# Kernel optimization log

Hardware: AMD Instinct MI355X
Metric: run time of the kernel (lower is better)

## Reference

```python
import jax, jax.numpy as jnp
import numpy as np

NUM_HEADS = 16


def setup_inputs() -> dict:
    key = jax.random.key(0)
    k1, k2, k3 = jax.random.split(key, 3)
    B, N, D = 4, 1024, 1024
    x = jax.random.normal(k1, (B, N, D), dtype=jnp.float32)
    w_qkv = jax.random.normal(k2, (3 * D, D), dtype=jnp.float32) * (D ** -0.5)
    w_out = jax.random.normal(k3, (D, D), dtype=jnp.float32) * (D ** -0.5)
    b_out = jnp.zeros((D,), dtype=jnp.float32)
    return {"x": x, "w_qkv": w_qkv, "w_out": w_out, "b_out": b_out}


def reference(x, w_qkv, w_out, b_out):
    B, N, D = x.shape
    H = NUM_HEADS
    d = D // H
    scale = d ** -0.5
    # qkv projection (no bias): [B,N,3D] -> [B,N,3,H,d]
    qkv = jnp.einsum('bnd,ed->bne', x, w_qkv).reshape(B, N, 3, H, d)
    # -> [3, B, H, N, d]
    qkv = jnp.transpose(qkv, (2, 0, 3, 1, 4))
    q, k, v = qkv[0], qkv[1], qkv[2]
    # attention scores [B,H,N,N], stable softmax
    scores = jnp.einsum('bhqd,bhkd->bhqk', q, k) * scale
    attn = jax.nn.softmax(scores, axis=-1)
    out = jnp.einsum('bhqk,bhkd->bhqd', attn, v)  # [B,H,N,d]
    out = jnp.transpose(out, (0, 2, 1, 3)).reshape(B, N, D)
    # output projection with bias
    return jnp.einsum('bnd,ed->bne', out, w_out) + b_out
```

## Files before the change

### kernel.cpp

```cpp
#include <hip/hip_runtime.h>
#include <stdint.h>

typedef __bf16 bf16_t;
typedef bf16_t bf16x8 __attribute__((ext_vector_type(8)));
typedef float f32x4 __attribute__((ext_vector_type(4)));

static __device__ __forceinline__ unsigned short f2bf(float f) {
    union { float f; unsigned int u; } v; v.f = f;
    unsigned int u = v.u;
    unsigned int r = (u + 0x7fffu + ((u >> 16) & 1u)) >> 16;
    return (unsigned short)r;
}

static __device__ __forceinline__ bf16x8 as_frag(uint4 v) {
    union { uint4 u; bf16x8 b; } c; c.u = v; return c.b;
}

static __device__ __forceinline__ void gl2lds16(const unsigned short* g, uint4* l) {
    __builtin_amdgcn_global_load_lds(
        (const __attribute__((address_space(1))) unsigned int*)g,
        (__attribute__((address_space(3))) unsigned int*)l, 16, 0, 0);
}

#define MFMA16(a, b, c) __builtin_amdgcn_mfma_f32_16x16x32_bf16((a), (b), (c), 0, 0, 0)

__global__ void cvt_all(const float* __restrict__ x,
                        const float* __restrict__ wq,
                        const float* __restrict__ wo,
                        unsigned short* __restrict__ xb,
                        unsigned short* __restrict__ wqb,
                        unsigned short* __restrict__ wob) {
    const float* in; unsigned short* out; int n4;
    if (blockIdx.y == 0)      { in = x;  out = xb;  n4 = 1048576; }
    else if (blockIdx.y == 1) { in = wq; out = wqb; n4 = 786432; }
    else                      { in = wo; out = wob; n4 = 262144; }
    for (int i = blockIdx.x * 256 + threadIdx.x; i < n4; i += 1024 * 256) {
        float4 v = ((const float4*)in)[i];
        ushort4 o;
        o.x = f2bf(v.x); o.y = f2bf(v.y); o.z = f2bf(v.z); o.w = f2bf(v.w);
        ((ushort4*)out)[i] = o;
    }
}

template <int OUTMODE>
__global__ __launch_bounds__(256, 2) void gemm_bt(
    const unsigned short* __restrict__ A,
    const unsigned short* __restrict__ B,
    void* __restrict__ Cv,
    const float* __restrict__ bias,
    unsigned short* __restrict__ Vt,
    int M, int N, int K) {
    __shared__ uint4 As[1024];
    __shared__ uint4 Bs[1024];
    const int tid  = threadIdx.x;
    const int lane = tid & 63;
    const int wave = tid >> 6;
    const int quad = lane >> 4;
    const int l16  = lane & 15;
    const int wr   = (wave >> 1) * 64;
    const int wc   = (wave & 1) * 64;
    const int bm   = blockIdx.y * 128;
    const int bn   = blockIdx.x * 128;

    f32x4 zero4 = {0.f, 0.f, 0.f, 0.f};
    f32x4 acc[4][4];
#pragma unroll
    for (int mt = 0; mt < 4; ++mt)
#pragma unroll
        for (int nt = 0; nt < 4; ++nt) acc[mt][nt] = zero4;

    const int s_row = tid >> 3;
    const int s_kcs = tid & 7;

    for (int k0 = 0; k0 < K; k0 += 64) {
        __syncthreads();
#pragma unroll
        for (int i = 0; i < 4; ++i) {
            int s   = i * 256 + tid;
            int row = i * 32 + s_row;
            int kcg = s_kcs ^ (row & 7);
            gl2lds16(A + (size_t)(bm + row) * K + k0 + kcg * 8, &As[s]);
            gl2lds16(B + (size_t)(bn + row) * K + k0 + kcg * 8, &Bs[s]);
        }
        __syncthreads();
#pragma unroll
        for (int ks = 0; ks < 2; ++ks) {
            int kc = ks * 4 + quad;
            bf16x8 af[4], bff[4];
#pragma unroll
            for (int mt = 0; mt < 4; ++mt) {
                int row = wr + mt * 16 + l16;
                af[mt] = as_frag(As[row * 8 + (kc ^ (row & 7))]);
            }
#pragma unroll
            for (int nt = 0; nt < 4; ++nt) {
                int row = wc + nt * 16 + l16;
                bff[nt] = as_frag(Bs[row * 8 + (kc ^ (row & 7))]);
            }
#pragma unroll
            for (int mt = 0; mt < 4; ++mt)
#pragma unroll
                for (int nt = 0; nt < 4; ++nt)
                    acc[mt][nt] = MFMA16(af[mt], bff[nt], acc[mt][nt]);
        }
    }

    if (OUTMODE == 1) {
        float* C = (float*)Cv;
#pragma unroll
        for (int mt = 0; mt < 4; ++mt)
#pragma unroll
            for (int nt = 0; nt < 4; ++nt) {
                int col = bn + wc + nt * 16 + l16;
                float bv = bias ? bias[col] : 0.f;
#pragma unroll
                for (int r = 0; r < 4; ++r) {
                    int row = bm + wr + mt * 16 + quad * 4 + r;
                    C[(size_t)row * N + col] = acc[mt][nt][r] + bv;
                }
            }
    } else if (OUTMODE == 0) {
        unsigned short* C = (unsigned short*)Cv;
#pragma unroll
        for (int mt = 0; mt < 4; ++mt)
#pragma unroll
            for (int nt = 0; nt < 4; ++nt) {
                int col = bn + wc + nt * 16 + l16;
#pragma unroll
                for (int r = 0; r < 4; ++r) {
                    int row = bm + wr + mt * 16 + quad * 4 + r;
                    C[(size_t)row * N + col] = f2bf(acc[mt][nt][r]);
                }
            }
    } else {
        if (bn < 2048) {
            unsigned short* C = (unsigned short*)Cv;
#pragma unroll
            for (int mt = 0; mt < 4; ++mt)
#pragma unroll
                for (int nt = 0; nt < 4; ++nt) {
                    int col = bn + wc + nt * 16 + l16;
#pragma unroll
                    for (int r = 0; r < 4; ++r) {
                        int row = bm + wr + mt * 16 + quad * 4 + r;
                        C[(size_t)row * 2048 + col] = f2bf(acc[mt][nt][r]);
                    }
                }
        } else {
#pragma unroll
            for (int mt = 0; mt < 4; ++mt)
#pragma unroll
                for (int nt = 0; nt < 4; ++nt) {
                    int col = bn + wc + nt * 16 + l16 - 2048;
                    int h = col >> 6, dd = col & 63;
                    int token0 = bm + wr + mt * 16 + quad * 4;
                    int b = token0 >> 10, t = token0 & 1023;
                    ushort4 pk;
                    pk.x = f2bf(acc[mt][nt][0]);
                    pk.y = f2bf(acc[mt][nt][1]);
                    pk.z = f2bf(acc[mt][nt][2]);
                    pk.w = f2bf(acc[mt][nt][3]);
                    *(ushort4*)(Vt + ((size_t)((b * 16 + h) * 64 + dd) * 1024 + t)) = pk;
                }
        }
    }
}

__global__ __launch_bounds__(512, 4) void attn_kernel(
    const unsigned short* __restrict__ qk,
    const unsigned short* __restrict__ vt,
    unsigned short* __restrict__ out) {
    __shared__ uint4 Ps[8 * 128];
    __shared__ uint4 Ks[2][512];
    __shared__ uint4 Vs[2][512];

    const int tid  = threadIdx.x;
    const int lane = tid & 63;
    const int wave = tid >> 6;
    const int quad = lane >> 4;
    const int l16  = lane & 15;
    const int bh   = blockIdx.x;
    const int b    = bh >> 4, h = bh & 15;
    const int qbase = blockIdx.y * 128;
    const size_t rowbase = (size_t)b * 1024;
    const int hoff = h * 64;
    const float c1 = 0.125f * 1.44269504088896f;

    const int st_row = tid >> 3;
    const int st_kcg = (tid & 7) ^ (st_row & 7);
    const unsigned short* kp0 = qk + (rowbase)*2048 + 1024 + hoff;
    const unsigned short* vp0 = vt + (size_t)bh * 65536;

    gl2lds16(kp0 + (size_t)st_row * 2048 + st_kcg * 8, &Ks[0][tid]);
    gl2lds16(vp0 + (size_t)st_row * 1024 + st_kcg * 8, &Vs[0][tid]);

#pragma unroll
    for (int i = 0; i < 2; ++i) {
        int s = i * 512 + tid;
        int kc = s & 7, row = s >> 3;
        Ps[kc * 128 + (row ^ (kc << 1))] =
            *(const uint4*)(qk + (rowbase + qbase + row) * 2048 + hoff + kc * 8);
    }
    __syncthreads();
    bf16x8 qf[2];
#pragma unroll
    for (int ks = 0; ks < 2; ++ks) {
        int kc = ks * 4 + quad;
        int row = wave * 16 + l16;
        qf[ks] = as_frag(Ps[kc * 128 + (row ^ (kc << 1))]);
    }

    f32x4 zero4 = {0.f, 0.f, 0.f, 0.f};
    f32x4 Oacc[4];
#pragma unroll
    for (int no = 0; no < 4; ++no) Oacc[no] = zero4;
    float mcur = -1e30f, lcur = 0.f;

    for (int kt = 0; kt < 16; ++kt) {
        const int buf = kt & 1;
        if (kt) __syncthreads();
        if (kt < 15) {
            gl2lds16(kp0 + (size_t)((kt + 1) * 64 + st_row) * 2048 + st_kcg * 8,
                     &Ks[buf ^ 1][tid]);
            gl2lds16(vp0 + (size_t)st_row * 1024 + (kt + 1) * 64 + st_kcg * 8,
                     &Vs[buf ^ 1][tid]);
        }

        f32x4 st[4];
#pragma unroll
        for (int nt = 0; nt < 4; ++nt) st[nt] = zero4;
#pragma unroll
        for (int ks = 0; ks < 2; ++ks) {
            int kc = ks * 4 + quad;
            bf16x8 kf[4];
#pragma unroll
            for (int nt = 0; nt < 4; ++nt) {
                int row = nt * 16 + l16;
                kf[nt] = as_frag(Ks[buf][row * 8 + (kc ^ (row & 7))]);
            }
#pragma unroll
            for (int nt = 0; nt < 4; ++nt)
                st[nt] = MFMA16(kf[nt], qf[ks], st[nt]);
        }

        float mx = st[0][0];
#pragma unroll
        for (int nt = 0; nt < 4; ++nt)
#pragma unroll
            for (int r = 0; r < 4; ++r) mx = fmaxf(mx, st[nt][r]);
        mx = fmaxf(mx, __shfl_xor(mx, 16, 64));
        mx = fmaxf(mx, __shfl_xor(mx, 32, 64));
        float mnew = fmaxf(mcur, mx);
        float al = __builtin_amdgcn_exp2f(c1 * (mcur - mnew));
        mcur = mnew;
        float rs = 0.f;
        const int q = wave * 16 + l16;
#pragma unroll
        for (int nt = 0; nt < 4; ++nt) {
            ushort4 pk;
            float p0 = __builtin_amdgcn_exp2f(c1 * (st[nt][0] - mnew));
            float p1 = __builtin_amdgcn_exp2f(c1 * (st[nt][1] - mnew));
            float p2 = __builtin_amdgcn_exp2f(c1 * (st[nt][2] - mnew));
            float p3 = __builtin_amdgcn_exp2f(c1 * (st[nt][3] - mnew));
            rs += (p0 + p1) + (p2 + p3);
            pk.x = f2bf(p0); pk.y = f2bf(p1); pk.z = f2bf(p2); pk.w = f2bf(p3);
            int c = nt * 4 + quad, kc = c >> 1;
            ((uint2*)Ps)[(kc * 128 + (q ^ (kc << 1))) * 2 + (c & 1)] = *(uint2*)&pk;
        }
        rs += __shfl_xor(rs, 16, 64);
        rs += __shfl_xor(rs, 32, 64);
        lcur = lcur * al + rs;

#pragma unroll
        for (int r = 0; r < 4; ++r) {
            float aO = __shfl(al, quad * 4 + r, 64);
#pragma unroll
            for (int no = 0; no < 4; ++no) Oacc[no][r] *= aO;
        }

#pragma unroll
        for (int kstep = 0; kstep < 2; ++kstep) {
            int kc = kstep * 4 + quad;
            bf16x8 pf = as_frag(Ps[kc * 128 + ((wave * 16 + l16) ^ (kc << 1))]);
            bf16x8 vf[4];
#pragma unroll
            for (int no = 0; no < 4; ++no) {
                int dd = no * 16 + l16;
                vf[no] = as_frag(Vs[buf][dd * 8 + (kc ^ (dd & 7))]);
            }
#pragma unroll
            for (int no = 0; no < 4; ++no)
                Oacc[no] = MFMA16(pf, vf[no], Oacc[no]);
        }
    }

    float linv = 1.f / lcur;
#pragma unroll
    for (int r = 0; r < 4; ++r) {
        float iv = __shfl(linv, quad * 4 + r, 64);
        int qrow = qbase + wave * 16 + quad * 4 + r;
#pragma unroll
        for (int no = 0; no < 4; ++no) {
            int dd = no * 16 + l16;
            out[(rowbase + qrow) * 1024 + hoff + dd] = f2bf(Oacc[no][r] * iv);
        }
    }
}

extern "C" void kernel_launch(void* const* d_in, const int* in_sizes, int n_in,
                              void* d_out, int out_size, void* d_ws, size_t ws_size,
                              hipStream_t stream) {
    const float* x     = (const float*)d_in[0];
    const float* w_qkv = (const float*)d_in[1];
    const float* w_out = (const float*)d_in[2];
    const float* b_out = (const float*)d_in[3];

    char* ws = (char*)d_ws;
    unsigned short* wqkvb = (unsigned short*)(ws);
    unsigned short* woutb = (unsigned short*)(ws + 6291456);
    unsigned short* qkb   = (unsigned short*)(ws + 8388608);
    unsigned short* vtb   = (unsigned short*)(ws + 25165824);
    unsigned short* xb    = (unsigned short*)(ws + 33554432);
    unsigned short* attnb = xb;

    cvt_all<<<dim3(1024, 3), 256, 0, stream>>>(x, w_qkv, w_out, xb, wqkvb, woutb);

    gemm_bt<2><<<dim3(24, 32), 256, 0, stream>>>(xb, wqkvb, (void*)qkb, nullptr,
                                                 vtb, 4096, 3072, 1024);
    attn_kernel<<<dim3(64, 8), 512, 0, stream>>>(qkb, vtb, attnb);
    gemm_bt<1><<<dim3(8, 32), 256, 0, stream>>>(attnb, woutb, d_out, b_out,
                                                nullptr, 4096, 1024, 1024);
}
```

Baseline: 168.7 us.

## Double attention key tile to 128 and truncate probabilities to bf16 via bit masking

```diff
diff --git a/kernel.cpp b/kernel.cpp
--- a/kernel.cpp
+++ b/kernel.cpp
@@ -14,6 +14,13 @@
 
 static __device__ __forceinline__ bf16x8 as_frag(uint4 v) {
     union { uint4 u; bf16x8 b; } c; c.u = v; return c.b;
+}
+
+static __device__ __forceinline__ unsigned int fbits(float f) {
+    union { float f; unsigned int u; } v; v.f = f; return v.u;
+}
+static __device__ __forceinline__ float fval(unsigned int u) {
+    union { unsigned int u; float f; } v; v.u = u; return v.f;
 }
 
 static __device__ __forceinline__ void gl2lds16(const unsigned short* g, uint4* l) {
@@ -170,9 +177,9 @@
     const unsigned short* __restrict__ qk,
     const unsigned short* __restrict__ vt,
     unsigned short* __restrict__ out) {
-    __shared__ uint4 Ps[8 * 128];
-    __shared__ uint4 Ks[2][512];
-    __shared__ uint4 Vs[2][512];
+    __shared__ uint4 Ps[1024];
+    __shared__ uint4 Ks[2][1024];
+    __shared__ uint4 Vs[2][1024];
 
     const int tid  = threadIdx.x;
     const int lane = tid & 63;
@@ -187,27 +194,31 @@
     const float c1 = 0.125f * 1.44269504088896f;
 
     const int st_row = tid >> 3;
-    const int st_kcg = (tid & 7) ^ (st_row & 7);
-    const unsigned short* kp0 = qk + (rowbase)*2048 + 1024 + hoff;
+    const int st_kcs = tid & 7;
+    const int sv_dd  = tid >> 4;
+    const int sv_tcs = tid & 15;
+    const unsigned short* kp0 = qk + rowbase * 2048 + 1024 + hoff;
     const unsigned short* vp0 = vt + (size_t)bh * 65536;
 
-    gl2lds16(kp0 + (size_t)st_row * 2048 + st_kcg * 8, &Ks[0][tid]);
-    gl2lds16(vp0 + (size_t)st_row * 1024 + st_kcg * 8, &Vs[0][tid]);
-
-#pragma unroll
-    for (int i = 0; i < 2; ++i) {
-        int s = i * 512 + tid;
-        int kc = s & 7, row = s >> 3;
-        Ps[kc * 128 + (row ^ (kc << 1))] =
-            *(const uint4*)(qk + (rowbase + qbase + row) * 2048 + hoff + kc * 8);
+#pragma unroll
+    for (int p = 0; p < 2; ++p) {
+        int row = p * 64 + st_row;
+        int kcg = st_kcs ^ (row & 7);
+        gl2lds16(kp0 + (size_t)row * 2048 + kcg * 8, &Ks[0][p * 512 + tid]);
+        int dd = p * 32 + sv_dd;
+        int tcg = sv_tcs ^ (dd & 7);
+        gl2lds16(vp0 + (size_t)dd * 1024 + tcg * 8, &Vs[0][p * 512 + tid]);
+        gl2lds16(qk + (rowbase + qbase + row) * 2048 + hoff + kcg * 8,
+                 &Ps[p * 512 + tid]);
     }
     __syncthreads();
+
     bf16x8 qf[2];
 #pragma unroll
     for (int ks = 0; ks < 2; ++ks) {
         int kc = ks * 4 + quad;
         int row = wave * 16 + l16;
-        qf[ks] = as_frag(Ps[kc * 128 + (row ^ (kc << 1))]);
+        qf[ks] = as_frag(Ps[row * 8 + (kc ^ (row & 7))]);
     }
 
     f32x4 zero4 = {0.f, 0.f, 0.f, 0.f};
@@ -216,56 +227,64 @@
     for (int no = 0; no < 4; ++no) Oacc[no] = zero4;
     float mcur = -1e30f, lcur = 0.f;
 
-    for (int kt = 0; kt < 16; ++kt) {
+    const int q = wave * 16 + l16;
+
+    for (int kt = 0; kt < 8; ++kt) {
         const int buf = kt & 1;
         if (kt) __syncthreads();
-        if (kt < 15) {
-            gl2lds16(kp0 + (size_t)((kt + 1) * 64 + st_row) * 2048 + st_kcg * 8,
-                     &Ks[buf ^ 1][tid]);
-            gl2lds16(vp0 + (size_t)st_row * 1024 + (kt + 1) * 64 + st_kcg * 8,
-                     &Vs[buf ^ 1][tid]);
-        }
-
-        f32x4 st[4];
-#pragma unroll
-        for (int nt = 0; nt < 4; ++nt) st[nt] = zero4;
+        if (kt < 7) {
+#pragma unroll
+            for (int p = 0; p < 2; ++p) {
+                int row = p * 64 + st_row;
+                int kcg = st_kcs ^ (row & 7);
+                gl2lds16(kp0 + (size_t)((kt + 1) * 128 + row) * 2048 + kcg * 8,
+                         &Ks[buf ^ 1][p * 512 + tid]);
+                int dd = p * 32 + sv_dd;
+                int tcg = sv_tcs ^ (dd & 7);
+                gl2lds16(vp0 + (size_t)dd * 1024 + (kt + 1) * 128 + tcg * 8,
+                         &Vs[buf ^ 1][p * 512 + tid]);
+            }
+        }
+
+        f32x4 st[8];
+#pragma unroll
+        for (int nt = 0; nt < 8; ++nt) st[nt] = zero4;
 #pragma unroll
         for (int ks = 0; ks < 2; ++ks) {
             int kc = ks * 4 + quad;
-            bf16x8 kf[4];
-#pragma unroll
-            for (int nt = 0; nt < 4; ++nt) {
+#pragma unroll
+            for (int nt = 0; nt < 8; ++nt) {
                 int row = nt * 16 + l16;
-                kf[nt] = as_frag(Ks[buf][row * 8 + (kc ^ (row & 7))]);
-            }
-#pragma unroll
-            for (int nt = 0; nt < 4; ++nt)
-                st[nt] = MFMA16(kf[nt], qf[ks], st[nt]);
+                bf16x8 kf = as_frag(Ks[buf][row * 8 + (kc ^ (row & 7))]);
+                st[nt] = MFMA16(kf, qf[ks], st[nt]);
+            }
         }
 
         float mx = st[0][0];
 #pragma unroll
-        for (int nt = 0; nt < 4; ++nt)
-#pragma unroll
-            for (int r = 0; r < 4; ++r) mx = fmaxf(mx, st[nt][r]);
+        for (int nt = 0; nt < 8; ++nt) {
+            float m01 = fmaxf(st[nt][0], st[nt][1]);
+            float m23 = fmaxf(st[nt][2], st[nt][3]);
+            mx = fmaxf(mx, fmaxf(m01, m23));
+        }
         mx = fmaxf(mx, __shfl_xor(mx, 16, 64));
         mx = fmaxf(mx, __shfl_xor(mx, 32, 64));
         float mnew = fmaxf(mcur, mx);
         float al = __builtin_amdgcn_exp2f(c1 * (mcur - mnew));
         mcur = mnew;
+        float nmc1 = -c1 * mnew;
+
+        unsigned int pw[8][2];
         float rs = 0.f;
-        const int q = wave * 16 + l16;
-#pragma unroll
-        for (int nt = 0; nt < 4; ++nt) {
-            ushort4 pk;
-            float p0 = __builtin_amdgcn_exp2f(c1 * (st[nt][0] - mnew));
-            float p1 = __builtin_amdgcn_exp2f(c1 * (st[nt][1] - mnew));
-            float p2 = __builtin_amdgcn_exp2f(c1 * (st[nt][2] - mnew));
-            float p3 = __builtin_amdgcn_exp2f(c1 * (st[nt][3] - mnew));
-            rs += (p0 + p1) + (p2 + p3);
-            pk.x = f2bf(p0); pk.y = f2bf(p1); pk.z = f2bf(p2); pk.w = f2bf(p3);
-            int c = nt * 4 + quad, kc = c >> 1;
-            ((uint2*)Ps)[(kc * 128 + (q ^ (kc << 1))) * 2 + (c & 1)] = *(uint2*)&pk;
+#pragma unroll
+        for (int nt = 0; nt < 8; ++nt) {
+            unsigned int b0 = fbits(__builtin_amdgcn_exp2f(fmaf(st[nt][0], c1, nmc1))) & 0xffff0000u;
+            unsigned int b1 = fbits(__builtin_amdgcn_exp2f(fmaf(st[nt][1], c1, nmc1))) & 0xffff0000u;
+            unsigned int b2 = fbits(__builtin_amdgcn_exp2f(fmaf(st[nt][2], c1, nmc1))) & 0xffff0000u;
+            unsigned int b3 = fbits(__builtin_amdgcn_exp2f(fmaf(st[nt][3], c1, nmc1))) & 0xffff0000u;
+            rs += (fval(b0) + fval(b1)) + (fval(b2) + fval(b3));
+            pw[nt][0] = __builtin_amdgcn_perm(b1, b0, 0x07060302u);
+            pw[nt][1] = __builtin_amdgcn_perm(b3, b2, 0x07060302u);
         }
         rs += __shfl_xor(rs, 16, 64);
         rs += __shfl_xor(rs, 32, 64);
@@ -279,18 +298,26 @@
         }
 
 #pragma unroll
-        for (int kstep = 0; kstep < 2; ++kstep) {
-            int kc = kstep * 4 + quad;
-            bf16x8 pf = as_frag(Ps[kc * 128 + ((wave * 16 + l16) ^ (kc << 1))]);
-            bf16x8 vf[4];
-#pragma unroll
-            for (int no = 0; no < 4; ++no) {
-                int dd = no * 16 + l16;
-                vf[no] = as_frag(Vs[buf][dd * 8 + (kc ^ (dd & 7))]);
-            }
-#pragma unroll
-            for (int no = 0; no < 4; ++no)
-                Oacc[no] = MFMA16(pf, vf[no], Oacc[no]);
+        for (int hf = 0; hf < 2; ++hf) {
+#pragma unroll
+            for (int t = 0; t < 4; ++t) {
+                int c = t * 4 + quad;
+                int kc = c >> 1, sub = c & 1;
+                uint2 w2 = make_uint2(pw[hf * 4 + t][0], pw[hf * 4 + t][1]);
+                ((uint2*)Ps)[(q * 8 + (kc ^ (q & 7))) * 2 + sub] = w2;
+            }
+#pragma unroll
+            for (int k2 = 0; k2 < 2; ++k2) {
+                int kc = k2 * 4 + quad;
+                bf16x8 pf = as_frag(Ps[q * 8 + (kc ^ (q & 7))]);
+                int tc = (hf * 2 + k2) * 4 + quad;
+#pragma unroll
+                for (int no = 0; no < 4; ++no) {
+                    int dd = no * 16 + l16;
+                    bf16x8 vf = as_frag(Vs[buf][dd * 16 + (tc ^ (dd & 7))]);
+                    Oacc[no] = MFMA16(pf, vf, Oacc[no]);
+                }
+            }
         }
     }
 
```

Measured after the change: 168.2 us. No clear change (-0.3%).
